# Kernel optimization log

Measured on AMD Instinct MI355X. Metric: run time of the kernel, lower is better.

The kernel has to match this reference:

```python
import jax, jax.numpy as jnp
import numpy as np

B, S, D = 4, 512, 2048
N_HEADS, N_KV, HEAD_DIM = 16, 4, 128
N_REP = N_HEADS // N_KV
FFN = 5632
E, TOPK, R = 8, 2, 16
LORA_SCALE = 32.0 / R  # alpha / r
EPS = 1e-5


def setup_inputs() -> dict:
    key = jax.random.key(0)
    ks = jax.random.split(key, 32)

    def p(k, shape, s=0.02):
        return jax.random.normal(k, shape, jnp.float32) * s

    data = jax.random.normal(ks[0], (B, S, D), jnp.float32)
    # causal additive mask [1,1,S,S]
    causal = jnp.tril(jnp.ones((S, S), jnp.bool_))
    mask = jnp.where(causal, 0.0, -1e9).astype(jnp.float32)[None, None]
    # rotary angles (llama interleaved pairing), half head_dim
    inv_freq = 1.0 / (10000.0 ** (np.arange(0, HEAD_DIM, 2, dtype=np.float32) / HEAD_DIM))
    angles = jnp.asarray(np.arange(S, dtype=np.float32)[:, None] * inv_freq[None, :])
    rope_cos = jnp.cos(angles)  # [S, HEAD_DIM//2]
    rope_sin = jnp.sin(angles)

    inp = dict(
        data=data, mask=mask, rope_cos=rope_cos, rope_sin=rope_sin,
        att_norm_w=jnp.ones((D,), jnp.float32),
        ffn_norm_w=jnp.ones((D,), jnp.float32),
        wq=p(ks[1], (D, D)), wk=p(ks[2], (N_KV * HEAD_DIM, D)),
        wv=p(ks[3], (N_KV * HEAD_DIM, D)), wo=p(ks[4], (D, D)),
        lqA=p(ks[5], (R, D)), lqB=p(ks[6], (D, R)),
        lkA=p(ks[7], (R, D)), lkB=p(ks[8], (N_KV * HEAD_DIM, R)),
        lvA=p(ks[9], (R, D)), lvB=p(ks[10], (N_KV * HEAD_DIM, R)),
        loA=p(ks[11], (R, D)), loB=p(ks[12], (D, R)),
        w1=p(ks[13], (FFN, D)), w2=p(ks[14], (D, FFN)), w3=p(ks[15], (FFN, D)),
        gate_w=p(ks[16], (E, D)),
        eA1=p(ks[17], (E, R, D)), eB1=p(ks[18], (E, FFN, R)),
        eA2=p(ks[19], (E, R, FFN)), eB2=p(ks[20], (E, D, R)),
        eA3=p(ks[21], (E, R, D)), eB3=p(ks[22], (E, FFN, R)),
    )
    return inp


def rmsnorm(x, w):
    return x * jax.lax.rsqrt(jnp.mean(x * x, axis=-1, keepdims=True) + EPS) * w


def lora_linear(x, W, A, Bm):
    # torch Linear weight is [out, in]; lora: x @ A^T @ B^T * scale
    return x @ W.T + ((x @ A.T) @ Bm.T) * LORA_SCALE


def apply_rope(x, cos, sin):
    # x: [B,S,H,Dh]; interleaved complex rotation per pair
    x1, x2 = x[..., 0::2], x[..., 1::2]
    c = cos[None, :, None, :]
    s = sin[None, :, None, :]
    o1 = x1 * c - x2 * s
    o2 = x1 * s + x2 * c
    return jnp.stack([o1, o2], axis=-1).reshape(x.shape)


def transformer_fwd(data, mask, rope_cos, rope_sin, att_norm_w, ffn_norm_w,
                    wq, wk, wv, wo, lqA, lqB, lkA, lkB, lvA, lvB, loA, loB,
                    w1, w2, w3, gate_w, eA1, eB1, eA2, eB2, eA3, eB3):
    b, s, _ = data.shape
    h = rmsnorm(data, att_norm_w)
    xq = lora_linear(h, wq, lqA, lqB).reshape(b, s, N_HEADS, HEAD_DIM)
    xk = lora_linear(h, wk, lkA, lkB).reshape(b, s, N_KV, HEAD_DIM)
    xv = lora_linear(h, wv, lvA, lvB).reshape(b, s, N_KV, HEAD_DIM)
    xq = apply_rope(xq, rope_cos, rope_sin)
    xk = apply_rope(xk, rope_cos, rope_sin)
    # repeat_kv: each kv head repeated n_rep times consecutively
    xk = jnp.repeat(xk, N_REP, axis=2)
    xv = jnp.repeat(xv, N_REP, axis=2)
    scores = jnp.einsum('bshd,bthd->bhst', xq, xk) / jnp.sqrt(jnp.float32(HEAD_DIM))
    scores = scores + mask
    attn = jax.nn.softmax(scores, axis=-1)
    out = jnp.einsum('bhst,bthd->bshd', attn, xv).reshape(b, s, D)
    data = data + lora_linear(out, wo, loA, loB)

    # MoE FFN (MixLoRA): shared base w1/w2/w3 + per-expert LoRA, top-k routing
    hn = rmsnorm(data, ffn_norm_w)
    x = hn.reshape(b * s, D)
    logits = x @ gate_w.T                       # [T, E]
    probs = jax.nn.softmax(logits, axis=-1)
    vals, idx = jax.lax.top_k(probs, TOPK)      # [T, k]
    vals = vals / jnp.sum(vals, axis=-1, keepdims=True)
    T = b * s
    route = jnp.zeros((T, E), x.dtype).at[jnp.arange(T)[:, None], idx].set(vals)
    h1 = x @ w1.T   # shared base projections
    h3 = x @ w3.T
    acc = jnp.zeros((T, D), x.dtype)
    for e in range(E):
        g1 = h1 + ((x @ eA1[e].T) @ eB1[e].T) * LORA_SCALE
        g3 = h3 + ((x @ eA3[e].T) @ eB3[e].T) * LORA_SCALE
        gh = jax.nn.silu(g1) * g3
        oe = gh @ w2.T + ((gh @ eA2[e].T) @ eB2[e].T) * LORA_SCALE
        acc = acc + route[:, e:e + 1] * oe
    return data + acc.reshape(b, s, D)


def reference(data, mask, rope_cos, rope_sin, att_norm_w, ffn_norm_w,
              wq, wk, wv, wo, lqA, lqB, lkA, lkB, lvA, lvB, loA, loB,
              w1, w2, w3, gate_w, eA1, eB1, eA2, eB2, eA3, eB3):
    return transformer_fwd(data, mask, rope_cos, rope_sin, att_norm_w, ffn_norm_w,
                           wq, wk, wv, wo, lqA, lqB, lkA, lkB, lvA, lvB, loA, loB,
                           w1, w2, w3, gate_w, eA1, eB1, eA2, eB2, eA3, eB3)
```

## Files before the change

kernel.cpp:

```cpp
#include <hip/hip_runtime.h>
#include <stdint.h>

#define DI static __device__ __forceinline__

typedef __attribute__((ext_vector_type(8))) short bf16x8;
typedef __attribute__((ext_vector_type(4))) float floatx4;

DI unsigned short f2bf(float x){
  unsigned int u = __float_as_uint(x);
  u += 0x7fffu + ((u >> 16) & 1u);
  return (unsigned short)(u >> 16);
}
DI float bf2f(unsigned short h){ return __uint_as_float(((unsigned int)h) << 16); }

#define GLOAD16(gp, lp) \
  __builtin_amdgcn_global_load_lds((const __attribute__((address_space(1))) unsigned int*)(gp), \
                                   (__attribute__((address_space(3))) unsigned int*)(lp), 16, 0, 0)

template<int OUTM, int RESM, bool CSKIP, bool SPLIT>
__global__ __launch_bounds__(256, 2)
void k_gemm(const unsigned short* __restrict__ A, long lda, long sA1, long sA2, long aLo,
            const unsigned short* __restrict__ B, long ldb, long sB1, long sB2, long bLo,
            void* __restrict__ C, long ldc, long sC1, long sC2, long cLo,
            const void* __restrict__ Rz, long ldr,
            const unsigned short* __restrict__ G1p, const float* __restrict__ ewp, int slot,
            int kIters, int zshift, int bshift)
{
  if (CSKIP && blockIdx.y > blockIdx.x) return;
  __shared__ __attribute__((aligned(16))) unsigned short As[SPLIT ? 8192 : 4096];
  __shared__ __attribute__((aligned(16))) unsigned short Bs[SPLIT ? 8192 : 4096];
  const int tid = threadIdx.x;
  const int w = tid >> 6, lane = tid & 63;
  const int wm = (w >> 1) * 64, wn = (w & 1) * 64;
  const int z = blockIdx.z;
  const int zr = z & ((1 << zshift) - 1);
  const int zb = z >> zshift;
  long k0 = 0;
  if (OUTM == 2 || OUTM == 8) k0 = (long)zb * (long)kIters * 32;
  const unsigned short* Ab = A + (long)((OUTM==8)?0:zb) * sA2 + (long)zr * sA1 + (long)blockIdx.x * 128 * lda + k0;
  const unsigned short* Bb = B + (long)((OUTM==8)?0:zb) * sB2 + (long)(zr >> bshift) * sB1 + (long)blockIdx.y * 128 * ldb + k0;

  const int rlo = w * 16 + (lane & 15);
  const int rhi = 64 + rlo;
  const int cc  = (lane >> 4) * 8;
  unsigned short* ldsA0 = As + w * 512;
  unsigned short* ldsA1 = As + 2048 + w * 512;
  unsigned short* ldsB0 = Bs + w * 512;
  unsigned short* ldsB1 = Bs + 2048 + w * 512;

  floatx4 acc[4][4];
  floatx4 zv = {0.f, 0.f, 0.f, 0.f};
#pragma unroll
  for (int i = 0; i < 4; ++i)
#pragma unroll
    for (int j = 0; j < 4; ++j) acc[i][j] = zv;

  const int abase = (wm >> 4) * 512 + lane * 8;
  const int bbase = (wn >> 4) * 512 + lane * 8;

  for (int kt = 0; kt < kIters; ++kt) {
    const unsigned short* pa = Ab + (long)kt * 32;
    const unsigned short* pb = Bb + (long)kt * 32;
    GLOAD16(pa + (long)rlo * lda + cc, ldsA0);
    GLOAD16(pa + (long)rhi * lda + cc, ldsA1);
    GLOAD16(pb + (long)rlo * ldb + cc, ldsB0);
    GLOAD16(pb + (long)rhi * ldb + cc, ldsB1);
    if (SPLIT) {
      const unsigned short* pal = pa + aLo;
      const unsigned short* pbl = pb + bLo;
      GLOAD16(pal + (long)rlo * lda + cc, As + 4096 + w * 512);
      GLOAD16(pal + (long)rhi * lda + cc, As + 6144 + w * 512);
      GLOAD16(pbl + (long)rlo * ldb + cc, Bs + 4096 + w * 512);
      GLOAD16(pbl + (long)rhi * ldb + cc, Bs + 6144 + w * 512);
    }
    __syncthreads();
    bf16x8 af[4], bfr[4];
#pragma unroll
    for (int i = 0; i < 4; ++i)
      af[i] = *(const bf16x8*)(As + abase + i * 512);
#pragma unroll
    for (int j = 0; j < 4; ++j)
      bfr[j] = *(const bf16x8*)(Bs + bbase + j * 512);
    if (SPLIT) {
      bf16x8 al[4], bl[4];
#pragma unroll
      for (int i = 0; i < 4; ++i)
        al[i] = *(const bf16x8*)(As + 4096 + abase + i * 512);
#pragma unroll
      for (int j = 0; j < 4; ++j)
        bl[j] = *(const bf16x8*)(Bs + 4096 + bbase + j * 512);
#pragma unroll
      for (int i = 0; i < 4; ++i)
#pragma unroll
        for (int j = 0; j < 4; ++j) {
          acc[i][j] = __builtin_amdgcn_mfma_f32_16x16x32_bf16(af[i], bfr[j], acc[i][j], 0, 0, 0);
          acc[i][j] = __builtin_amdgcn_mfma_f32_16x16x32_bf16(af[i], bl[j], acc[i][j], 0, 0, 0);
          acc[i][j] = __builtin_amdgcn_mfma_f32_16x16x32_bf16(al[i], bfr[j], acc[i][j], 0, 0, 0);
        }
    } else {
#pragma unroll
      for (int i = 0; i < 4; ++i)
#pragma unroll
        for (int j = 0; j < 4; ++j)
          acc[i][j] = __builtin_amdgcn_mfma_f32_16x16x32_bf16(af[i], bfr[j], acc[i][j], 0, 0, 0);
    }
    __syncthreads();
  }

  const long mb = (long)blockIdx.x * 128 + wm + ((lane >> 4) * 4);
  const long nb = (long)blockIdx.y * 128 + wn + (lane & 15);
  const long cbase = (long)zb * sC2 + (long)zr * sC1;
#pragma unroll
  for (int i = 0; i < 4; ++i) {
#pragma unroll
    for (int j = 0; j < 4; ++j) {
#pragma unroll
      for (int rr = 0; rr < 4; ++rr) {
        long m = mb + i * 16 + rr;
        long n = nb + j * 16;
        float v = acc[i][j][rr];
        if (RESM == 1) v += ((const float*)Rz)[m * ldr + n];
        if (RESM == 2) v += bf2f(((const unsigned short*)Rz)[m * ldr + n]);
        if (OUTM == 0 || OUTM == 8) ((float*)C)[cbase + m * ldc + n] = v;
        else if (OUTM == 1) ((unsigned short*)C)[cbase + m * ldc + n] = f2bf(v);
        else if (OUTM == 2) atomicAdd((float*)C + cbase + m * ldc + n, v);
        else if (OUTM == 4) {
          float g1 = bf2f(G1p[m * ldc + n]);
          float s1 = g1 / (1.f + __expf(-g1));
          ((unsigned short*)C)[cbase + m * ldc + n] = f2bf(ewp[m * 2 + slot] * s1 * v);
        } else if (OUTM == 5) {
          unsigned short h = f2bf(v);
          unsigned short l = f2bf(v - bf2f(h));
          ((unsigned short*)C)[cbase + m * ldc + n] = h;
          ((unsigned short*)C)[cbase + m * ldc + n + cLo] = l;
        } else {
          long bq = m >> 9, sI = m & 511, kv = n >> 7, dI = n & 127;
          long t = (((bq * 4 + kv) * 128 + dI) << 9) + sI;
          unsigned short h = f2bf(v);
          unsigned short l = f2bf(v - bf2f(h));
          ((unsigned short*)C)[t] = h;
          ((unsigned short*)C)[t + cLo] = l;
        }
      }
    }
  }
}

__global__ void k_rmsnorm(const float* __restrict__ x, const float* __restrict__ w,
                          unsigned short* __restrict__ ob, long loOff){
  int t = blockIdx.x;
  const float* row = x + (size_t)t * 2048;
  float ss = 0.f;
  for (int i = threadIdx.x; i < 2048; i += 256){ float v = row[i]; ss += v * v; }
#pragma unroll
  for (int o = 32; o; o >>= 1) ss += __shfl_xor(ss, o);
  __shared__ float sred[4]; __shared__ float srms;
  int lane = threadIdx.x & 63, wid = threadIdx.x >> 6;
  if (lane == 0) sred[wid] = ss;
  __syncthreads();
  if (threadIdx.x == 0) srms = rsqrtf((sred[0]+sred[1]+sred[2]+sred[3]) * (1.f/2048.f) + 1e-5f);
  __syncthreads();
  float rr = srms;
  for (int i = threadIdx.x; i < 2048; i += 256){
    float v = row[i] * rr * w[i];
    unsigned short h = f2bf(v);
    ob[(size_t)t * 2048 + i] = h;
    if (loOff) ob[(size_t)t * 2048 + i + loOff] = f2bf(v - bf2f(h));
  }
}

__global__ void k_fold(const float* __restrict__ W, const float* __restrict__ Bm,
                       const float* __restrict__ A, unsigned short* __restrict__ out, long loOff){
  int idx = blockIdx.x * 256 + threadIdx.x;
  int n = idx >> 11, k = idx & 2047;
  float acc = W[idx];
  const float* br = Bm + (size_t)n * 16;
#pragma unroll
  for (int r = 0; r < 16; ++r) acc += 2.0f * br[r] * A[r * 2048 + k];
  unsigned short h = f2bf(acc);
  out[idx] = h;
  out[idx + loOff] = f2bf(acc - bf2f(h));
}

__global__ void k_cvt4(const float* __restrict__ in, unsigned short* __restrict__ out){
  int i = (blockIdx.x * 256 + threadIdx.x) * 4;
  float4 v = *(const float4*)(in + i);
  unsigned long long pk = (unsigned long long)f2bf(v.x)
    | ((unsigned long long)f2bf(v.y) << 16)
    | ((unsigned long long)f2bf(v.z) << 32)
    | ((unsigned long long)f2bf(v.w) << 48);
  *(unsigned long long*)(out + i) = pk;
}

__global__ void k_beff(const float* __restrict__ eB, unsigned short* __restrict__ out, int F){
  int idx = blockIdx.x * 256 + threadIdx.x;
  int f = idx >> 7, er = idx & 127;
  int e = er >> 4, r = er & 15;
  out[idx] = f2bf(eB[((size_t)e * F + f) * 16 + r]);
}

__global__ void k_qkv_epi(const float* __restrict__ P,
                          const float* __restrict__ rc, const float* __restrict__ rs,
                          unsigned short* __restrict__ qb, unsigned short* __restrict__ kb,
                          unsigned short* __restrict__ vT){
  int idx = blockIdx.x * 256 + threadIdx.x;
  int t = idx / 1536, p = idx - t * 1536;
  int c = p * 2;
  const float2 a = *(const float2*)(P + (size_t)t * 3072 + c);
  const float2 b = *(const float2*)(P + 6291456 + (size_t)t * 3072 + c);
  float v0 = a.x + b.x, v1 = a.y + b.y;
  int s = t & 511;
  if (c < 2560) {
    int i = (c & 127) >> 1;
    float co = rc[s * 64 + i], sn = rs[s * 64 + i];
    float o0 = v0 * co - v1 * sn;
    float o1 = v0 * sn + v1 * co;
    v0 = o0; v1 = o1;
  }
  unsigned short h0 = f2bf(v0), l0 = f2bf(v0 - bf2f(h0));
  unsigned short h1 = f2bf(v1), l1 = f2bf(v1 - bf2f(h1));
  if (c < 2048) {
    size_t o = (size_t)t * 2048 + c;
    qb[o] = h0; qb[o + 1] = h1;
    qb[o + 4194304] = l0; qb[o + 4194305] = l1;
  } else if (c < 2560) {
    size_t o = (size_t)t * 512 + (c - 2048);
    kb[o] = h0; kb[o + 1] = h1;
    kb[o + 1048576] = l0; kb[o + 1048577] = l1;
  } else {
    int d = c - 2560;
    int kv = d >> 7, dI = d & 127, bq = t >> 9;
    size_t o = (((size_t)(bq * 4 + kv) * 128 + dI) << 9) + s;
    vT[o] = h0; vT[o + 512] = h1;
    vT[o + 1048576] = l0; vT[o + 1048576 + 512] = l1;
  }
}

__global__ void k_add2res(const float* __restrict__ P, const float* __restrict__ res,
                          float* __restrict__ out){
  int i = (blockIdx.x * 256 + threadIdx.x) * 4;
  float4 a = *(const float4*)(P + i);
  float4 b = *(const float4*)(P + 4194304 + i);
  float4 r = *(const float4*)(res + i);
  float4 o; o.x = a.x + b.x + r.x; o.y = a.y + b.y + r.y;
  o.z = a.z + b.z + r.z; o.w = a.w + b.w + r.w;
  *(float4*)(out + i) = o;
}

__global__ void k_softmax(float* __restrict__ sp){
  int row = blockIdx.x;
  int s = row & 511;
  float* in = sp + (size_t)row * 512;
  unsigned short* op = (unsigned short*)in;
  int t0 = threadIdx.x, t1 = threadIdx.x + 256;
  const float scale = 0.088388347648318447f;
  float v0 = (t0 <= s) ? in[t0] * scale : -3.0e38f;
  float v1 = (t1 <= s) ? in[t1] * scale : -3.0e38f;
  float mx = fmaxf(v0, v1);
#pragma unroll
  for (int o = 32; o; o >>= 1) mx = fmaxf(mx, __shfl_xor(mx, o));
  __shared__ float sred[8];
  int lane = threadIdx.x & 63, wid = threadIdx.x >> 6;
  if (lane == 0) sred[wid] = mx;
  __syncthreads();
  mx = fmaxf(fmaxf(sred[0], sred[1]), fmaxf(sred[2], sred[3]));
  float e0 = (t0 <= s) ? __expf(v0 - mx) : 0.f;
  float e1 = (t1 <= s) ? __expf(v1 - mx) : 0.f;
  float sum = e0 + e1;
#pragma unroll
  for (int o = 32; o; o >>= 1) sum += __shfl_xor(sum, o);
  if (lane == 0) sred[4 + wid] = sum;
  __syncthreads();
  sum = sred[4] + sred[5] + sred[6] + sred[7];
  float inv = 1.f / sum;
  float p0 = e0 * inv, p1 = e1 * inv;
  unsigned short h0 = f2bf(p0), h1 = f2bf(p1);
  op[t0] = h0; op[512 + t0] = f2bf(p0 - bf2f(h0));
  op[t1] = h1; op[512 + t1] = f2bf(p1 - bf2f(h1));
}

__global__ void k_route(const float* __restrict__ x2, const float* __restrict__ w,
                        const float* __restrict__ gw, int* __restrict__ eidx,
                        float* __restrict__ ew){
  int t = blockIdx.x; int lane = threadIdx.x;
  const float* row = x2 + (size_t)t * 2048;
  float ss = 0.f;
  for (int d = lane; d < 2048; d += 64){ float v = row[d]; ss += v * v; }
#pragma unroll
  for (int o = 32; o; o >>= 1) ss += __shfl_xor(ss, o);
  float rr = rsqrtf(ss * (1.f/2048.f) + 1e-5f);
  float acc[8] = {0,0,0,0,0,0,0,0};
  for (int d = lane; d < 2048; d += 64){
    float xv = row[d] * rr * w[d];
#pragma unroll
    for (int e = 0; e < 8; ++e) acc[e] += xv * gw[e * 2048 + d];
  }
#pragma unroll
  for (int e = 0; e < 8; ++e)
#pragma unroll
    for (int o = 32; o; o >>= 1) acc[e] += __shfl_xor(acc[e], o);
  if (lane == 0){
    int i0 = 0;
#pragma unroll
    for (int e = 1; e < 8; ++e) if (acc[e] > acc[i0]) i0 = e;
    int i1 = -1;
#pragma unroll
    for (int e = 0; e < 8; ++e) if (e != i0 && (i1 < 0 || acc[e] > acc[i1])) i1 = e;
    float p1 = __expf(acc[i1] - acc[i0]);
    float inv = 1.f / (1.f + p1);
    eidx[t * 2 + 0] = i0; eidx[t * 2 + 1] = i1;
    ew[t * 2 + 0] = inv;  ew[t * 2 + 1] = p1 * inv;
  }
}

__global__ void k_zero(float* __restrict__ p){
  p[(size_t)blockIdx.x * 256 + threadIdx.x] = 0.f;
}

__global__ void k_ubuild(const float* __restrict__ U1, const float* __restrict__ U3,
                         const int* __restrict__ eidx,
                         unsigned short* __restrict__ u10, unsigned short* __restrict__ u11,
                         unsigned short* __restrict__ u30, unsigned short* __restrict__ u31){
  int idx = blockIdx.x * 256 + threadIdx.x;
  int t = idx >> 7, j = idx & 127; int e = j >> 4;
  int e0 = eidx[t * 2], e1 = eidx[t * 2 + 1];
  float v1 = U1[idx] * 2.0f, v3 = U3[idx] * 2.0f;
  u10[idx] = (e == e0) ? f2bf(v1) : (unsigned short)0;
  u11[idx] = (e == e1) ? f2bf(v1) : (unsigned short)0;
  u30[idx] = (e == e0) ? f2bf(v3) : (unsigned short)0;
  u31[idx] = (e == e1) ? f2bf(v3) : (unsigned short)0;
}

__global__ void k_addip(unsigned short* __restrict__ a, const unsigned short* __restrict__ b){
  size_t i = (size_t)blockIdx.x * 256 + threadIdx.x;
  a[i] = f2bf(bf2f(a[i]) + bf2f(b[i]));
}

__global__ void k_vhat(const float* __restrict__ U20, const float* __restrict__ U21,
                       const int* __restrict__ eidx, unsigned short* __restrict__ out){
  int idx = blockIdx.x * 256 + threadIdx.x;
  int t = idx >> 7, j = idx & 127; int e = j >> 4;
  int e0 = eidx[t * 2], e1 = eidx[t * 2 + 1];
  float v = 0.f;
  if (e == e0) v = 2.0f * U20[idx];
  else if (e == e1) v = 2.0f * U21[idx];
  out[idx] = f2bf(v);
}

extern "C" void kernel_launch(void* const* d_in, const int* in_sizes, int n_in,
                              void* d_out, int out_size, void* d_ws, size_t ws_size,
                              hipStream_t stream){
  const float* data  = (const float*)d_in[0];
  const float* rcos  = (const float*)d_in[2];
  const float* rsin  = (const float*)d_in[3];
  const float* attw  = (const float*)d_in[4];
  const float* ffnw  = (const float*)d_in[5];
  const float* wq    = (const float*)d_in[6];
  const float* wk    = (const float*)d_in[7];
  const float* wv    = (const float*)d_in[8];
  const float* wo    = (const float*)d_in[9];
  const float* lqA   = (const float*)d_in[10];
  const float* lqB   = (const float*)d_in[11];
  const float* lkA   = (const float*)d_in[12];
  const float* lkB   = (const float*)d_in[13];
  const float* lvA   = (const float*)d_in[14];
  const float* lvB   = (const float*)d_in[15];
  const float* loA   = (const float*)d_in[16];
  const float* loB   = (const float*)d_in[17];
  const float* w1    = (const float*)d_in[18];
  const float* w2    = (const float*)d_in[19];
  const float* w3    = (const float*)d_in[20];
  const float* gatew = (const float*)d_in[21];
  const float* eA1   = (const float*)d_in[22];
  const float* eB1   = (const float*)d_in[23];
  const float* eA2   = (const float*)d_in[24];
  const float* eB2   = (const float*)d_in[25];
  const float* eA3   = (const float*)d_in[26];
  const float* eB3   = (const float*)d_in[27];
  (void)in_sizes; (void)n_in; (void)out_size; (void)ws_size;

  char* base = (char*)d_ws;
  float* data2 = (float*)d_out;

  unsigned short* hb   = (unsigned short*)(base + 0);
  unsigned short* Wqkv = (unsigned short*)(base + 16777216);
  float*          QKVf = (float*)(base + 41943040);
  unsigned short* qb   = (unsigned short*)(base + 92274688);
  unsigned short* kb   = (unsigned short*)(base + 109051904);
  unsigned short* vT   = (unsigned short*)(base + 113246208);
  float*          sc   = (float*)(base + 0);
  unsigned short* scU  = (unsigned short*)(base + 0);
  unsigned short* ao   = (unsigned short*)(base + 67108864);
  unsigned short* Wo   = (unsigned short*)(base + 0);
  float*          Wof  = (float*)(base + 16777216);

  size_t off = 0;
  auto alloc = [&](size_t n)->char*{ char* p = base + off; off = (off + n + 255) & ~(size_t)255; return p; };
  int*   eidx = (int*)alloc(16384);
  float* ew   = (float*)alloc(16384);
  unsigned short* hnb  = (unsigned short*)alloc(8388608);
  unsigned short* h1b  = (unsigned short*)alloc(23068672);
  unsigned short* h3b  = (unsigned short*)alloc(23068672);
  unsigned short* wbuf = (unsigned short*)alloc(23068672);
  unsigned short* gh0  = (unsigned short*)alloc(23068672);
  unsigned short* eA1c = (unsigned short*)alloc(524288);
  unsigned short* eA3c = (unsigned short*)alloc(524288);
  unsigned short* eA2c = (unsigned short*)alloc(1441792);
  unsigned short* Bf1  = (unsigned short*)alloc(1441792);
  unsigned short* Bf3  = (unsigned short*)alloc(1441792);
  unsigned short* Bf2  = (unsigned short*)alloc(524288);
  float* Uz = (float*)alloc(4194304);
  float* U1 = Uz, *U3 = Uz + 262144, *U20 = Uz + 524288, *U21 = Uz + 786432;
  unsigned short* Ut10 = (unsigned short*)alloc(524288);
  unsigned short* Ut11 = (unsigned short*)alloc(524288);
  unsigned short* Ut30 = (unsigned short*)alloc(524288);
  unsigned short* Ut31 = (unsigned short*)alloc(524288);
  unsigned short* vhat = (unsigned short*)alloc(524288);
  unsigned short* gh1  = h1b;
  float*          W2f  = (float*)h1b;

  k_rmsnorm<<<2048, 256, 0, stream>>>(data, attw, hb, 4194304);
  k_fold<<<16384, 256, 0, stream>>>(wq, lqB, lqA, Wqkv, 6291456);
  k_fold<<<4096, 256, 0, stream>>>(wk, lkB, lkA, Wqkv + 4194304, 6291456);
  k_fold<<<4096, 256, 0, stream>>>(wv, lvB, lvA, Wqkv + 5242880, 6291456);

  k_gemm<8,0,false,true><<<dim3(16,24,2), 256, 0, stream>>>(
      hb,2048,0,0,4194304, Wqkv,2048,0,0,6291456,
      QKVf, 3072, 0, 6291456, 0, nullptr,0, nullptr,nullptr,0, 32, 0, 0);
  k_qkv_epi<<<12288, 256, 0, stream>>>(QKVf, rcos, rsin, qb, kb, vT);

  k_gemm<0,0,true,true><<<dim3(4,4,64), 256, 0, stream>>>(
      qb, 2048, 128, 1048576, 4194304, kb, 512, 128, 262144, 1048576,
      sc, 512, 262144, 4194304, 0, nullptr,0, nullptr,nullptr,0, 4, 4, 2);
  k_softmax<<<32768, 256, 0, stream>>>(sc);
  k_gemm<5,0,false,true><<<dim3(4,1,64), 256, 0, stream>>>(
      scU, 1024, 524288, 8388608, 512, vT, 512, 65536, 262144, 1048576,
      ao, 2048, 128, 1048576, 4194304, nullptr,0, nullptr,nullptr,0, 16, 4, 2);

  k_fold<<<16384, 256, 0, stream>>>(wo, loB, loA, Wo, 4194304);
  k_gemm<8,0,false,true><<<dim3(16,16,2), 256, 0, stream>>>(
      ao,2048,0,0,4194304, Wo,2048,0,0,4194304,
      Wof, 2048, 0, 4194304, 0, nullptr,0, nullptr,nullptr,0, 32, 0, 0);
  k_add2res<<<4096, 256, 0, stream>>>(Wof, data, data2);

  k_rmsnorm<<<2048, 256, 0, stream>>>(data2, ffnw, hnb, 0);
  k_route<<<2048, 64, 0, stream>>>(data2, ffnw, gatew, eidx, ew);

  k_cvt4<<<11264, 256, 0, stream>>>(w1, wbuf);
  k_gemm<1,0,false,false><<<dim3(16,44,1), 256, 0, stream>>>(
      hnb,2048,0,0,0, wbuf,2048,0,0,0, h1b,5632,0,0,0, nullptr,0, nullptr,nullptr,0, 64,0,0);
  k_cvt4<<<11264, 256, 0, stream>>>(w3, wbuf);
  k_gemm<1,0,false,false><<<dim3(16,44,1), 256, 0, stream>>>(
      hnb,2048,0,0,0, wbuf,2048,0,0,0, h3b,5632,0,0,0, nullptr,0, nullptr,nullptr,0, 64,0,0);

  k_cvt4<<<256, 256, 0, stream>>>(eA1, eA1c);
  k_cvt4<<<256, 256, 0, stream>>>(eA3, eA3c);
  k_cvt4<<<704, 256, 0, stream>>>(eA2, eA2c);
  k_beff<<<2816, 256, 0, stream>>>(eB1, Bf1, 5632);
  k_beff<<<2816, 256, 0, stream>>>(eB3, Bf3, 5632);
  k_beff<<<1024, 256, 0, stream>>>(eB2, Bf2, 2048);
  k_zero<<<4096, 256, 0, stream>>>(Uz);

  k_gemm<2,0,false,false><<<dim3(16,1,8), 256, 0, stream>>>(
      hnb,2048,0,0,0, eA1c,2048,0,0,0, U1,128,0,0,0, nullptr,0, nullptr,nullptr,0, 8,0,0);
  k_gemm<2,0,false,false><<<dim3(16,1,8), 256, 0, stream>>>(
      hnb,2048,0,0,0, eA3c,2048,0,0,0, U3,128,0,0,0, nullptr,0, nullptr,nullptr,0, 8,0,0);
  k_ubuild<<<1024, 256, 0, stream>>>(U1, U3, eidx, Ut10, Ut11, Ut30, Ut31);

  k_gemm<1,2,false,false><<<dim3(16,44,1), 256, 0, stream>>>(
      Ut10,128,0,0,0, Bf1,128,0,0,0, wbuf,5632,0,0,0, h1b,5632, nullptr,nullptr,0, 4,0,0);
  k_gemm<4,2,false,false><<<dim3(16,44,1), 256, 0, stream>>>(
      Ut30,128,0,0,0, Bf3,128,0,0,0, gh0,5632,0,0,0, h3b,5632, wbuf,ew,0, 4,0,0);
  k_gemm<2,0,false,false><<<dim3(16,1,8), 256, 0, stream>>>(
      gh0,5632,0,0,0, eA2c,5632,0,0,0, U20,128,0,0,0, nullptr,0, nullptr,nullptr,0, 22,0,0);
  k_gemm<1,2,false,false><<<dim3(16,44,1), 256, 0, stream>>>(
      Ut11,128,0,0,0, Bf1,128,0,0,0, wbuf,5632,0,0,0, h1b,5632, nullptr,nullptr,0, 4,0,0);
  k_gemm<4,2,false,false><<<dim3(16,44,1), 256, 0, stream>>>(
      Ut31,128,0,0,0, Bf3,128,0,0,0, gh1,5632,0,0,0, h3b,5632, wbuf,ew,1, 4,0,0);
  k_gemm<2,0,false,false><<<dim3(16,1,8), 256, 0, stream>>>(
      gh1,5632,0,0,0, eA2c,5632,0,0,0, U21,128,0,0,0, nullptr,0, nullptr,nullptr,0, 22,0,0);

  k_addip<<<45056, 256, 0, stream>>>(gh0, gh1);
  k_vhat<<<1024, 256, 0, stream>>>(U20, U21, eidx, vhat);
  k_gemm<2,0,false,false><<<dim3(16,16,1), 256, 0, stream>>>(
      vhat,128,0,0,0, Bf2,128,0,0,0, data2,2048,0,0,0, nullptr,0, nullptr,nullptr,0, 4,0,0);
  k_cvt4<<<11264, 256, 0, stream>>>(w2, wbuf);
  k_gemm<8,0,false,false><<<dim3(16,16,2), 256, 0, stream>>>(
      gh0,5632,0,0,0, wbuf,5632,0,0,0, W2f, 2048, 0, 4194304, 0,
      nullptr,0, nullptr,nullptr,0, 88,0,0);
  k_add2res<<<4096, 256, 0, stream>>>(W2f, data2, data2);
}
```

Baseline: 1.132 ms.

## Add 4-stage pipelined 512-thread GEMM kernel for dense projections

Introduces k_gemm2, a 512-thread GEMM that issues async global-to-LDS loads four stages deep and uses explicit vmcnt waits with one barrier per k-step. It also raises priority around the MFMA section and allows larger tiles (256x256, 128x256). The QKV, output, w1/w3 and w2 projections are switched to it. The aim is to hide memory latency and raise data reuse in the dominant dense GEMMs, at the cost of more LDS per block, which may reduce occupancy.

```diff
diff --git a/kernel.cpp b/kernel.cpp
--- a/kernel.cpp
+++ b/kernel.cpp
@@ -16,6 +16,8 @@
 #define GLOAD16(gp, lp) \
   __builtin_amdgcn_global_load_lds((const __attribute__((address_space(1))) unsigned int*)(gp), \
                                    (__attribute__((address_space(3))) unsigned int*)(lp), 16, 0, 0)
+
+#define WAITVM(n) asm volatile("s_waitcnt vmcnt(" #n ")" ::: "memory")
 
 template<int OUTM, int RESM, bool CSKIP, bool SPLIT>
 __global__ __launch_bounds__(256, 2)
@@ -141,6 +143,149 @@
           ((unsigned short*)C)[t] = h;
           ((unsigned short*)C)[t + cLo] = l;
         }
+      }
+    }
+  }
+}
+
+template<int BM, int BN, bool SPLIT, int OUTM>
+__global__ __launch_bounds__(512, 2)
+void k_gemm2(const unsigned short* __restrict__ A, long lda, long aLo,
+             const unsigned short* __restrict__ B, long ldb, long bLo,
+             void* __restrict__ C, long ldc, long sC2, int kIters)
+{
+  constexpr int DEPTH = 4;
+  constexpr int ASZ = BM * 32 * (SPLIT ? 2 : 1);
+  constexpr int BSZ = BN * 32 * (SPLIT ? 2 : 1);
+  constexpr int TSZ = ASZ + BSZ;
+  constexpr int FM = BM / 32, FN = BN / 64;
+  constexpr int LPT = (SPLIT ? 2 : 1) * (BM / 128 + BN / 128);
+  static_assert(LPT == 3 || LPT == 4, "vmcnt constants assume LPT in {3,4}");
+  __shared__ __attribute__((aligned(16))) unsigned short sm[DEPTH * TSZ];
+
+  const int tid = threadIdx.x;
+  const int w = tid >> 6, lane = tid & 63;
+  const int wm = (w >> 2) * (BM / 2), wn = (w & 3) * (BN / 4);
+  const int zb = blockIdx.z;
+  const long k0 = (OUTM == 8) ? (long)zb * (long)kIters * 32 : 0;
+  const unsigned short* Ab = A + (long)blockIdx.x * BM * lda + k0;
+  const unsigned short* Bb = B + (long)blockIdx.y * BN * ldb + k0;
+  const int rA = lane & 15;
+  const int cc = (lane >> 4) * 8;
+
+  floatx4 acc[FM][FN];
+  floatx4 zv = {0.f, 0.f, 0.f, 0.f};
+#pragma unroll
+  for (int i = 0; i < FM; ++i)
+#pragma unroll
+    for (int j = 0; j < FN; ++j) acc[i][j] = zv;
+
+  auto stage = [&](int kt) {
+    const unsigned short* pa = Ab + (long)kt * 32;
+    const unsigned short* pb = Bb + (long)kt * 32;
+    unsigned short* sa = sm + (size_t)(kt & (DEPTH - 1)) * TSZ;
+    unsigned short* sb = sa + ASZ;
+#pragma unroll
+    for (int r = 0; r < BM / 128; ++r) {
+      const int b = r * 8 + w;
+      const long row = b * 16 + rA;
+      GLOAD16(pa + row * lda + cc, sa + b * 512);
+      if (SPLIT) GLOAD16(pa + aLo + row * lda + cc, sa + BM * 32 + b * 512);
+    }
+#pragma unroll
+    for (int r = 0; r < BN / 128; ++r) {
+      const int b = r * 8 + w;
+      const long row = b * 16 + rA;
+      GLOAD16(pb + row * ldb + cc, sb + b * 512);
+      if (SPLIT) GLOAD16(pb + bLo + row * ldb + cc, sb + BN * 32 + b * 512);
+    }
+  };
+
+  auto waitpipe = [&](int ahead) {
+    if (LPT == 4) {
+      if (ahead >= 2) { WAITVM(8); }
+      else if (ahead == 1) { WAITVM(4); }
+      else { WAITVM(0); }
+    } else {
+      if (ahead >= 2) { WAITVM(6); }
+      else if (ahead == 1) { WAITVM(3); }
+      else { WAITVM(0); }
+    }
+  };
+
+  {
+    int np = DEPTH - 1; if (np > kIters) np = kIters;
+    for (int p = 0; p < np; ++p) stage(p);
+    __builtin_amdgcn_sched_barrier(0);
+    waitpipe(np - 1);
+    __builtin_amdgcn_s_barrier();
+  }
+
+  const int aoff = (wm >> 4) * 512 + lane * 8;
+  const int boff = (wn >> 4) * 512 + lane * 8;
+
+  for (int kt = 0; kt < kIters; ++kt) {
+    if (kt + DEPTH - 1 < kIters) stage(kt + DEPTH - 1);
+
+    const unsigned short* sa = sm + (size_t)(kt & (DEPTH - 1)) * TSZ;
+    const unsigned short* sb = sa + ASZ;
+    bf16x8 af[FM], bfr[FN];
+#pragma unroll
+    for (int i = 0; i < FM; ++i)
+      af[i] = *(const bf16x8*)(sa + aoff + i * 512);
+#pragma unroll
+    for (int j = 0; j < FN; ++j)
+      bfr[j] = *(const bf16x8*)(sb + boff + j * 512);
+    if (SPLIT) {
+      bf16x8 al[FM], bl[FN];
+#pragma unroll
+      for (int i = 0; i < FM; ++i)
+        al[i] = *(const bf16x8*)(sa + BM * 32 + aoff + i * 512);
+#pragma unroll
+      for (int j = 0; j < FN; ++j)
+        bl[j] = *(const bf16x8*)(sb + BN * 32 + boff + j * 512);
+      __builtin_amdgcn_s_setprio(1);
+#pragma unroll
+      for (int i = 0; i < FM; ++i)
+#pragma unroll
+        for (int j = 0; j < FN; ++j) {
+          acc[i][j] = __builtin_amdgcn_mfma_f32_16x16x32_bf16(af[i], bfr[j], acc[i][j], 0, 0, 0);
+          acc[i][j] = __builtin_amdgcn_mfma_f32_16x16x32_bf16(af[i], bl[j], acc[i][j], 0, 0, 0);
+          acc[i][j] = __builtin_amdgcn_mfma_f32_16x16x32_bf16(al[i], bfr[j], acc[i][j], 0, 0, 0);
+        }
+      __builtin_amdgcn_s_setprio(0);
+    } else {
+      __builtin_amdgcn_s_setprio(1);
+#pragma unroll
+      for (int i = 0; i < FM; ++i)
+#pragma unroll
+        for (int j = 0; j < FN; ++j)
+          acc[i][j] = __builtin_amdgcn_mfma_f32_16x16x32_bf16(af[i], bfr[j], acc[i][j], 0, 0, 0);
+      __builtin_amdgcn_s_setprio(0);
+    }
+
+    __builtin_amdgcn_sched_barrier(0);
+    int ahead = kIters - 2 - kt;
+    if (ahead > DEPTH - 2) ahead = DEPTH - 2;
+    if (ahead < 0) ahead = 0;
+    waitpipe(ahead);
+    __builtin_amdgcn_s_barrier();
+  }
+
+  const long mb = (long)blockIdx.x * BM + wm + ((lane >> 4) * 4);
+  const long nb = (long)blockIdx.y * BN + wn + (lane & 15);
+  const long cbase = (long)zb * sC2;
+#pragma unroll
+  for (int i = 0; i < FM; ++i) {
+#pragma unroll
+    for (int j = 0; j < FN; ++j) {
+#pragma unroll
+      for (int rr = 0; rr < 4; ++rr) {
+        long m = mb + i * 16 + rr;
+        long n = nb + j * 16;
+        float v = acc[i][j][rr];
+        if (OUTM == 8) ((float*)C)[cbase + m * ldc + n] = v;
+        else ((unsigned short*)C)[m * ldc + n] = f2bf(v);
       }
     }
   }
@@ -424,9 +569,8 @@
   k_fold<<<4096, 256, 0, stream>>>(wk, lkB, lkA, Wqkv + 4194304, 6291456);
   k_fold<<<4096, 256, 0, stream>>>(wv, lvB, lvA, Wqkv + 5242880, 6291456);
 
-  k_gemm<8,0,false,true><<<dim3(16,24,2), 256, 0, stream>>>(
-      hb,2048,0,0,4194304, Wqkv,2048,0,0,6291456,
-      QKVf, 3072, 0, 6291456, 0, nullptr,0, nullptr,nullptr,0, 32, 0, 0);
+  k_gemm2<128,128,true,8><<<dim3(16,24,2), 512, 0, stream>>>(
+      hb, 2048, 4194304, Wqkv, 2048, 6291456, QKVf, 3072, 6291456, 32);
   k_qkv_epi<<<12288, 256, 0, stream>>>(QKVf, rcos, rsin, qb, kb, vT);
 
   k_gemm<0,0,true,true><<<dim3(4,4,64), 256, 0, stream>>>(
@@ -438,20 +582,19 @@
       ao, 2048, 128, 1048576, 4194304, nullptr,0, nullptr,nullptr,0, 16, 4, 2);
 
   k_fold<<<16384, 256, 0, stream>>>(wo, loB, loA, Wo, 4194304);
-  k_gemm<8,0,false,true><<<dim3(16,16,2), 256, 0, stream>>>(
-      ao,2048,0,0,4194304, Wo,2048,0,0,4194304,
-      Wof, 2048, 0, 4194304, 0, nullptr,0, nullptr,nullptr,0, 32, 0, 0);
+  k_gemm2<128,128,true,8><<<dim3(16,16,2), 512, 0, stream>>>(
+      ao, 2048, 4194304, Wo, 2048, 4194304, Wof, 2048, 4194304, 32);
   k_add2res<<<4096, 256, 0, stream>>>(Wof, data, data2);
 
   k_rmsnorm<<<2048, 256, 0, stream>>>(data2, ffnw, hnb, 0);
   k_route<<<2048, 64, 0, stream>>>(data2, ffnw, gatew, eidx, ew);
 
   k_cvt4<<<11264, 256, 0, stream>>>(w1, wbuf);
-  k_gemm<1,0,false,false><<<dim3(16,44,1), 256, 0, stream>>>(
-      hnb,2048,0,0,0, wbuf,2048,0,0,0, h1b,5632,0,0,0, nullptr,0, nullptr,nullptr,0, 64,0,0);
+  k_gemm2<256,256,false,1><<<dim3(8,22,1), 512, 0, stream>>>(
+      hnb, 2048, 0, wbuf, 2048, 0, h1b, 5632, 0, 64);
   k_cvt4<<<11264, 256, 0, stream>>>(w3, wbuf);
-  k_gemm<1,0,false,false><<<dim3(16,44,1), 256, 0, stream>>>(
-      hnb,2048,0,0,0, wbuf,2048,0,0,0, h3b,5632,0,0,0, nullptr,0, nullptr,nullptr,0, 64,0,0);
+  k_gemm2<256,256,false,1><<<dim3(8,22,1), 512, 0, stream>>>(
+      hnb, 2048, 0, wbuf, 2048, 0, h3b, 5632, 0, 64);
 
   k_cvt4<<<256, 256, 0, stream>>>(eA1, eA1c);
   k_cvt4<<<256, 256, 0, stream>>>(eA3, eA3c);
@@ -485,8 +628,7 @@
   k_gemm<2,0,false,false><<<dim3(16,16,1), 256, 0, stream>>>(
       vhat,128,0,0,0, Bf2,128,0,0,0, data2,2048,0,0,0, nullptr,0, nullptr,nullptr,0, 4,0,0);
   k_cvt4<<<11264, 256, 0, stream>>>(w2, wbuf);
-  k_gemm<8,0,false,false><<<dim3(16,16,2), 256, 0, stream>>>(
-      gh0,5632,0,0,0, wbuf,5632,0,0,0, W2f, 2048, 0, 4194304, 0,
-      nullptr,0, nullptr,nullptr,0, 88,0,0);
+  k_gemm2<128,256,false,8><<<dim3(16,8,2), 512, 0, stream>>>(
+      gh0, 5632, 0, wbuf, 5632, 0, W2f, 2048, 4194304, 88);
   k_add2res<<<4096, 256, 0, stream>>>(W2f, data2, data2);
 }
```

New measurement: 1.058 ms. 1.07x faster.
